# Kernel optimization log

Measured on AMD Instinct MI355X. Metric: run time of the kernel, lower is better.

## Reference

```python
import jax, jax.numpy as jnp
import numpy as np

N = 8192
EPS = 1e-6


def setup_inputs() -> dict:
    key = jax.random.key(0)
    k1, k2, k3, k4 = jax.random.split(key, 4)
    P_risk = jax.random.normal(k1, (N,), dtype=jnp.float32)
    P_surv = jax.random.normal(k2, (N,), dtype=jnp.float32)
    T = jax.random.uniform(k3, (N,), dtype=jnp.float32)
    E = jax.random.randint(k4, (N,), 0, 2, dtype=jnp.int32)
    return {"P_risk": P_risk, "P_surv": P_surv, "T": T, "E": E}


def _compute_loss(P, M, E_eff):
    # P: [N] log-hazards, M: [N, N] float mask, E_eff: [N] effective event weights
    P_exp = jnp.exp(P)
    # sum_j M[i, j] * exp(P[j])  -- masked risk-set sum as a matvec
    P_exp_sum = M @ P_exp
    log_ratio = jnp.log(P_exp / (P_exp_sum + EPS))
    return -jnp.sum(log_ratio * E_eff) / jnp.sum(E_eff)


def reference(P_risk, P_surv, T, E):
    Ef = E.astype(jnp.float32)
    # M_risk[i, j] = 1 if T[i] < T[j]
    M_risk = (T[:, None] < T[None, :]).astype(jnp.float32)
    # M_surv[i, j] = 1 if T[i] > T[j] and E[j] == 1
    M_surv = (T[:, None] > T[None, :]).astype(jnp.float32) * Ef[None, :]

    # mode='risk': E * (row of M_risk nonempty)
    E_risk = Ef * (jnp.sum(M_risk, axis=1) > 0).astype(jnp.float32)
    # mode='surv': just (row of M_surv nonempty)
    E_surv = (jnp.sum(M_surv, axis=1) > 0).astype(jnp.float32)

    loss_risk = _compute_loss(P_risk, M_risk, E_risk)
    loss_surv = _compute_loss(P_surv, M_surv, E_surv)
    return (loss_risk, loss_surv)
```

## Files before the change

kernel.cpp:

```cpp
#include <hip/hip_runtime.h>
#include <math.h>

#define NN 8192
#define EPSF 1e-6f
#define R 8
#define GX (NN / R)


__global__ __launch_bounds__(256) void ds_main(
    const float* __restrict__ Pr, const float* __restrict__ Ps,
    const float* __restrict__ T,  const int* __restrict__ E,
    float4* __restrict__ part) {
  const int tid  = threadIdx.x;
  const int row0 = blockIdx.x * R;

  float Ti[R];
#pragma unroll
  for (int r = 0; r < R; ++r) Ti[r] = T[row0 + r];

  float sr[R], ss[R];
#pragma unroll
  for (int r = 0; r < R; ++r) { sr[r] = 0.0f; ss[r] = 0.0f; }

  for (int k = 0; k < NN; k += 1024) {
    const int j = k + tid * 4;
    float4 t4  = *(const float4*)(T  + j);
    float4 pr4 = *(const float4*)(Pr + j);
    float4 ps4 = *(const float4*)(Ps + j);
    int4   e4  = *(const int4*)(E  + j);
    float er0 = __expf(pr4.x), er1 = __expf(pr4.y),
          er2 = __expf(pr4.z), er3 = __expf(pr4.w);
    float es0 = e4.x ? __expf(ps4.x) : 0.0f;
    float es1 = e4.y ? __expf(ps4.y) : 0.0f;
    float es2 = e4.z ? __expf(ps4.z) : 0.0f;
    float es3 = e4.w ? __expf(ps4.w) : 0.0f;
#pragma unroll
    for (int r = 0; r < R; ++r) {
      bool g0 = t4.x > Ti[r];  sr[r] += g0 ? er0 : 0.0f;  ss[r] += g0 ? 0.0f : es0;
      bool g1 = t4.y > Ti[r];  sr[r] += g1 ? er1 : 0.0f;  ss[r] += g1 ? 0.0f : es1;
      bool g2 = t4.z > Ti[r];  sr[r] += g2 ? er2 : 0.0f;  ss[r] += g2 ? 0.0f : es2;
      bool g3 = t4.w > Ti[r];  sr[r] += g3 ? er3 : 0.0f;  ss[r] += g3 ? 0.0f : es3;
    }
  }

#pragma unroll
  for (int r = 0; r < R; ++r) {
    for (int off = 32; off > 0; off >>= 1) {
      sr[r] += __shfl_down(sr[r], off);
      ss[r] += __shfl_down(ss[r], off);
    }
  }
  __shared__ float sh[4][2 * R];
  const int wid = tid >> 6, lane = tid & 63;
  if (lane == 0) {
#pragma unroll
    for (int r = 0; r < R; ++r) { sh[wid][r] = sr[r]; sh[wid][R + r] = ss[r]; }
  }
  __syncthreads();
  __shared__ float fin[2 * R];
  if (tid < 2 * R)
    fin[tid] = sh[0][tid] + sh[1][tid] + sh[2][tid] + sh[3][tid];
  __syncthreads();

  float nr = 0.0f, dr = 0.0f, ns = 0.0f, nds = 0.0f;
  if (tid < R) {
    const int   row = row0 + tid;
    const int   e   = E[row];
    const float prv = Pr[row], psv = Ps[row];
    const float es_diag = e ? __expf(psv) : 0.0f;
    const float srv = fin[tid];
    const float ssv = fin[R + tid] - es_diag;
    const float wr = (e != 0 && srv > 0.0f) ? 1.0f : 0.0f;
    const float wsv = (ssv > 0.0f) ? 1.0f : 0.0f;
    nr  = wr  * (prv - logf(srv + EPSF));
    dr  = wr;
    ns  = wsv * (psv - logf(ssv + EPSF));
    nds = wsv;
  }
  if (tid < 64) {
#pragma unroll
    for (int off = R / 2; off > 0; off >>= 1) {
      nr  += __shfl_down(nr,  off);
      dr  += __shfl_down(dr,  off);
      ns  += __shfl_down(ns,  off);
      nds += __shfl_down(nds, off);
    }
    if (tid == 0) part[blockIdx.x] = make_float4(nr, dr, ns, nds);
  }
}

__global__ __launch_bounds__(256) void ds_finalize(
    const float4* __restrict__ part, float* __restrict__ out) {
  float nr = 0.0f, dr = 0.0f, ns = 0.0f, nds = 0.0f;
  for (int i = threadIdx.x; i < GX; i += 256) {
    float4 p = part[i];
    nr += p.x; dr += p.y; ns += p.z; nds += p.w;
  }
  for (int off = 32; off > 0; off >>= 1) {
    nr  += __shfl_down(nr,  off);
    dr  += __shfl_down(dr,  off);
    ns  += __shfl_down(ns,  off);
    nds += __shfl_down(nds, off);
  }
  __shared__ float sh[4][4];
  const int wid = threadIdx.x >> 6, lane = threadIdx.x & 63;
  if (lane == 0) {
    sh[0][wid] = nr; sh[1][wid] = dr; sh[2][wid] = ns; sh[3][wid] = nds;
  }
  __syncthreads();
  if (threadIdx.x == 0) {
    float NR = sh[0][0] + sh[0][1] + sh[0][2] + sh[0][3];
    float DR = sh[1][0] + sh[1][1] + sh[1][2] + sh[1][3];
    float NS = sh[2][0] + sh[2][1] + sh[2][2] + sh[2][3];
    float DS = sh[3][0] + sh[3][1] + sh[3][2] + sh[3][3];
    out[0] = -NR / DR;
    out[1] = -NS / DS;
  }
}

extern "C" void kernel_launch(void* const* d_in, const int* in_sizes, int n_in,
                              void* d_out, int out_size, void* d_ws, size_t ws_size,
                              hipStream_t stream) {
  const float* Pr = (const float*)d_in[0];
  const float* Ps = (const float*)d_in[1];
  const float* T  = (const float*)d_in[2];
  const int*   E  = (const int*)d_in[3];
  float* out = (float*)d_out;

  float4* part = (float4*)d_ws;

  ds_main<<<GX, 256, 0, stream>>>(Pr, Ps, T, E, part);
  ds_finalize<<<1, 256, 0, stream>>>(part, out);
}
```

Measured before the change: 73.70 us.

## Replace quadratic masked risk-set sums with single-block bucket sort and prefix scans

The O(N^2) pairwise comparison over all rows is replaced by one workgroup that buckets samples by T into shared memory. It builds per-bucket exp sums with LDS atomics, takes prefix and suffix scans over the buckets, and scatters the samples into bucket order. Each element then needs only the scanned totals plus an exact comparison against the other members of its own bucket. The final reduction is folded into the same kernel, so the second launch disappears. The cost is a single-block design that relies on T being roughly uniform in [0,1) for bucket balance. Skewed T would still give correct results but would serialise the within-bucket loops.

```diff
diff --git a/kernel.cpp b/kernel.cpp
--- a/kernel.cpp
+++ b/kernel.cpp
@@ -1,118 +1,171 @@
 #include <hip/hip_runtime.h>
 #include <math.h>
 
-#define NN 8192
+#define NN   8192
+#define K    1024
+#define NT   1024
+#define EPT  8
 #define EPSF 1e-6f
-#define R 8
-#define GX (NN / R)
 
 
-__global__ __launch_bounds__(256) void ds_main(
+__device__ __forceinline__ float wave_incl_scan_f(float x, int lane) {
+#pragma unroll
+  for (int off = 1; off < 64; off <<= 1) {
+    float y = __shfl_up(x, off);
+    if (lane >= off) x += y;
+  }
+  return x;
+}
+__device__ __forceinline__ unsigned wave_incl_scan_u(unsigned x, int lane) {
+#pragma unroll
+  for (int off = 1; off < 64; off <<= 1) {
+    unsigned y = __shfl_up(x, off);
+    if (lane >= off) x += y;
+  }
+  return x;
+}
+
+__device__ __forceinline__ float block_excl_scan_f(float v, float* wtmp, int tid) {
+  const int lane = tid & 63, wid = tid >> 6;
+  float incl = wave_incl_scan_f(v, lane);
+  if (lane == 63) wtmp[wid] = incl;
+  __syncthreads();
+  if (tid < 64) {
+    float w = (tid < 16) ? wtmp[tid] : 0.0f;
+    w = wave_incl_scan_f(w, lane);
+    if (tid < 16) wtmp[tid] = w;
+  }
+  __syncthreads();
+  float base = (wid > 0) ? wtmp[wid - 1] : 0.0f;
+  return base + incl - v;
+}
+__device__ __forceinline__ unsigned block_excl_scan_u(unsigned v, unsigned* wtmp, int tid) {
+  const int lane = tid & 63, wid = tid >> 6;
+  unsigned incl = wave_incl_scan_u(v, lane);
+  if (lane == 63) wtmp[wid] = incl;
+  __syncthreads();
+  if (tid < 64) {
+    unsigned w = (tid < 16) ? wtmp[tid] : 0u;
+    w = wave_incl_scan_u(w, lane);
+    if (tid < 16) wtmp[tid] = w;
+  }
+  __syncthreads();
+  unsigned base = (wid > 0) ? wtmp[wid - 1] : 0u;
+  return base + incl - v;
+}
+
+__global__ __launch_bounds__(NT) void ds_all(
     const float* __restrict__ Pr, const float* __restrict__ Ps,
     const float* __restrict__ T,  const int* __restrict__ E,
-    float4* __restrict__ part) {
+    float* __restrict__ out) {
+  __shared__ unsigned cnt[K];
+  __shared__ unsigned cur[K];
+  __shared__ float    bER[K];
+  __shared__ float    bES[K];
+  __shared__ float    sT[NN];
+  __shared__ float    sER[NN];
+  __shared__ float    sES[NN];
+  __shared__ float    wtmp[64];
+
   const int tid  = threadIdx.x;
-  const int row0 = blockIdx.x * R;
+  const int lane = tid & 63, wid = tid >> 6;
 
-  float Ti[R];
+  cnt[tid] = 0u; cur[tid] = 0u; bER[tid] = 0.0f; bES[tid] = 0.0f;
+  __syncthreads();
+
+  float t8[EPT], pr8[EPT], ps8[EPT], er8[EPT], es8[EPT];
+  int   ev8[EPT], b8[EPT];
+  {
+    const int j = tid * EPT;
+    float4 ta = *(const float4*)(T  + j), tb = *(const float4*)(T  + j + 4);
+    float4 pa = *(const float4*)(Pr + j), pb = *(const float4*)(Pr + j + 4);
+    float4 qa = *(const float4*)(Ps + j), qb = *(const float4*)(Ps + j + 4);
+    int4   ea = *(const int4*)(E + j),    eb = *(const int4*)(E + j + 4);
+    t8[0]=ta.x;  t8[1]=ta.y;  t8[2]=ta.z;  t8[3]=ta.w;
+    t8[4]=tb.x;  t8[5]=tb.y;  t8[6]=tb.z;  t8[7]=tb.w;
+    pr8[0]=pa.x; pr8[1]=pa.y; pr8[2]=pa.z; pr8[3]=pa.w;
+    pr8[4]=pb.x; pr8[5]=pb.y; pr8[6]=pb.z; pr8[7]=pb.w;
+    ps8[0]=qa.x; ps8[1]=qa.y; ps8[2]=qa.z; ps8[3]=qa.w;
+    ps8[4]=qb.x; ps8[5]=qb.y; ps8[6]=qb.z; ps8[7]=qb.w;
+    ev8[0]=ea.x; ev8[1]=ea.y; ev8[2]=ea.z; ev8[3]=ea.w;
+    ev8[4]=eb.x; ev8[5]=eb.y; ev8[6]=eb.z; ev8[7]=eb.w;
+  }
 #pragma unroll
-  for (int r = 0; r < R; ++r) Ti[r] = T[row0 + r];
+  for (int e = 0; e < EPT; ++e) {
+    er8[e] = __expf(pr8[e]);
+    es8[e] = ev8[e] ? __expf(ps8[e]) : 0.0f;
+    int b = (int)(t8[e] * (float)K);
+    b = min(max(b, 0), K - 1);
+    b8[e] = b;
+    atomicAdd(&cnt[b], 1u);
+    atomicAdd(&bER[b], er8[e]);
+    atomicAdd(&bES[b], es8[e]);
+  }
+  __syncthreads();
 
-  float sr[R], ss[R];
+  unsigned myc  = cnt[tid];
+  float    myes = bES[tid];
+  float    myerR = bER[K - 1 - tid];
+  __syncthreads();
+  unsigned startv = block_excl_scan_u(myc, (unsigned*)wtmp, tid);
+  __syncthreads();
+  float prees = block_excl_scan_f(myes, wtmp, tid);
+  __syncthreads();
+  float sufR = block_excl_scan_f(myerR, wtmp, tid);
+  __syncthreads();
+  cnt[tid] = startv;
+  bES[tid] = prees;
+  bER[K - 1 - tid] = sufR;
+  __syncthreads();
+
 #pragma unroll
-  for (int r = 0; r < R; ++r) { sr[r] = 0.0f; ss[r] = 0.0f; }
+  for (int e = 0; e < EPT; ++e) {
+    unsigned pos = cnt[b8[e]] + atomicAdd(&cur[b8[e]], 1u);
+    sT[pos]  = t8[e];
+    sER[pos] = er8[e];
+    sES[pos] = es8[e];
+  }
+  __syncthreads();
 
-  for (int k = 0; k < NN; k += 1024) {
-    const int j = k + tid * 4;
-    float4 t4  = *(const float4*)(T  + j);
-    float4 pr4 = *(const float4*)(Pr + j);
-    float4 ps4 = *(const float4*)(Ps + j);
-    int4   e4  = *(const int4*)(E  + j);
-    float er0 = __expf(pr4.x), er1 = __expf(pr4.y),
-          er2 = __expf(pr4.z), er3 = __expf(pr4.w);
-    float es0 = e4.x ? __expf(ps4.x) : 0.0f;
-    float es1 = e4.y ? __expf(ps4.y) : 0.0f;
-    float es2 = e4.z ? __expf(ps4.z) : 0.0f;
-    float es3 = e4.w ? __expf(ps4.w) : 0.0f;
+  float nr = 0.0f, dr = 0.0f, ns = 0.0f, nds = 0.0f;
 #pragma unroll
-    for (int r = 0; r < R; ++r) {
-      bool g0 = t4.x > Ti[r];  sr[r] += g0 ? er0 : 0.0f;  ss[r] += g0 ? 0.0f : es0;
-      bool g1 = t4.y > Ti[r];  sr[r] += g1 ? er1 : 0.0f;  ss[r] += g1 ? 0.0f : es1;
-      bool g2 = t4.z > Ti[r];  sr[r] += g2 ? er2 : 0.0f;  ss[r] += g2 ? 0.0f : es2;
-      bool g3 = t4.w > Ti[r];  sr[r] += g3 ? er3 : 0.0f;  ss[r] += g3 ? 0.0f : es3;
+  for (int e = 0; e < EPT; ++e) {
+    const int   b = b8[e];
+    const float t = t8[e];
+    float srv = bER[b];
+    float ssv = bES[b];
+    const unsigned p0 = cnt[b];
+    const unsigned p1 = (b == K - 1) ? (unsigned)NN : cnt[b + 1];
+    for (unsigned p = p0; p < p1; ++p) {
+      float tj = sT[p];
+      srv += (tj > t) ? sER[p] : 0.0f;
+      ssv += (tj < t) ? sES[p] : 0.0f;
     }
+    const float wr  = (ev8[e] != 0 && srv > 0.0f) ? 1.0f : 0.0f;
+    const float wsv = (ssv > 0.0f) ? 1.0f : 0.0f;
+    nr  += wr  * (pr8[e] - logf(srv + EPSF));
+    dr  += wr;
+    ns  += wsv * (ps8[e] - logf(ssv + EPSF));
+    nds += wsv;
   }
 
 #pragma unroll
-  for (int r = 0; r < R; ++r) {
-    for (int off = 32; off > 0; off >>= 1) {
-      sr[r] += __shfl_down(sr[r], off);
-      ss[r] += __shfl_down(ss[r], off);
-    }
-  }
-  __shared__ float sh[4][2 * R];
-  const int wid = tid >> 6, lane = tid & 63;
-  if (lane == 0) {
-#pragma unroll
-    for (int r = 0; r < R; ++r) { sh[wid][r] = sr[r]; sh[wid][R + r] = ss[r]; }
-  }
-  __syncthreads();
-  __shared__ float fin[2 * R];
-  if (tid < 2 * R)
-    fin[tid] = sh[0][tid] + sh[1][tid] + sh[2][tid] + sh[3][tid];
-  __syncthreads();
-
-  float nr = 0.0f, dr = 0.0f, ns = 0.0f, nds = 0.0f;
-  if (tid < R) {
-    const int   row = row0 + tid;
-    const int   e   = E[row];
-    const float prv = Pr[row], psv = Ps[row];
-    const float es_diag = e ? __expf(psv) : 0.0f;
-    const float srv = fin[tid];
-    const float ssv = fin[R + tid] - es_diag;
-    const float wr = (e != 0 && srv > 0.0f) ? 1.0f : 0.0f;
-    const float wsv = (ssv > 0.0f) ? 1.0f : 0.0f;
-    nr  = wr  * (prv - logf(srv + EPSF));
-    dr  = wr;
-    ns  = wsv * (psv - logf(ssv + EPSF));
-    nds = wsv;
-  }
-  if (tid < 64) {
-#pragma unroll
-    for (int off = R / 2; off > 0; off >>= 1) {
-      nr  += __shfl_down(nr,  off);
-      dr  += __shfl_down(dr,  off);
-      ns  += __shfl_down(ns,  off);
-      nds += __shfl_down(nds, off);
-    }
-    if (tid == 0) part[blockIdx.x] = make_float4(nr, dr, ns, nds);
-  }
-}
-
-__global__ __launch_bounds__(256) void ds_finalize(
-    const float4* __restrict__ part, float* __restrict__ out) {
-  float nr = 0.0f, dr = 0.0f, ns = 0.0f, nds = 0.0f;
-  for (int i = threadIdx.x; i < GX; i += 256) {
-    float4 p = part[i];
-    nr += p.x; dr += p.y; ns += p.z; nds += p.w;
-  }
   for (int off = 32; off > 0; off >>= 1) {
     nr  += __shfl_down(nr,  off);
     dr  += __shfl_down(dr,  off);
     ns  += __shfl_down(ns,  off);
     nds += __shfl_down(nds, off);
   }
-  __shared__ float sh[4][4];
-  const int wid = threadIdx.x >> 6, lane = threadIdx.x & 63;
   if (lane == 0) {
-    sh[0][wid] = nr; sh[1][wid] = dr; sh[2][wid] = ns; sh[3][wid] = nds;
+    wtmp[wid] = nr; wtmp[16 + wid] = dr; wtmp[32 + wid] = ns; wtmp[48 + wid] = nds;
   }
   __syncthreads();
-  if (threadIdx.x == 0) {
-    float NR = sh[0][0] + sh[0][1] + sh[0][2] + sh[0][3];
-    float DR = sh[1][0] + sh[1][1] + sh[1][2] + sh[1][3];
-    float NS = sh[2][0] + sh[2][1] + sh[2][2] + sh[2][3];
-    float DS = sh[3][0] + sh[3][1] + sh[3][2] + sh[3][3];
+  if (tid == 0) {
+    float NR = 0, DR = 0, NS = 0, DS = 0;
+#pragma unroll
+    for (int w = 0; w < 16; ++w) {
+      NR += wtmp[w]; DR += wtmp[16 + w]; NS += wtmp[32 + w]; DS += wtmp[48 + w];
+    }
     out[0] = -NR / DR;
     out[1] = -NS / DS;
   }
@@ -127,8 +180,5 @@
   const int*   E  = (const int*)d_in[3];
   float* out = (float*)d_out;
 
-  float4* part = (float4*)d_ws;
-
-  ds_main<<<GX, 256, 0, stream>>>(Pr, Ps, T, E, part);
-  ds_finalize<<<1, 256, 0, stream>>>(part, out);
+  ds_all<<<1, NT, 0, stream>>>(Pr, Ps, T, E, out);
 }
```

Result: slower. 99.81 us (+35.4%).

## Split column range across two blocks per row group and move log-loss to finalize

Applied to the files above, without the earlier changes.

Each 8-row group is now handled by two blocks, each covering half of the j columns, which doubles the grid from 1024 to 2048 blocks. Per-row partial risk and survival sums go to workspace arrays. A 1024-thread finalize kernel then adds the two halves per row, subtracts the diagonal term, and computes the log-loss terms and reductions. The aim is more parallelism and occupancy (launch bounds now request 8 blocks per CU). In exchange the per-row log work moves into a single-block finalize pass that reads 4x8192 extra floats, and each block redoes the exp work for its half.

```diff
diff --git a/kernel.cpp b/kernel.cpp
--- a/kernel.cpp
+++ b/kernel.cpp
@@ -1,18 +1,24 @@
 #include <hip/hip_runtime.h>
 #include <math.h>
 
-#define NN 8192
+#define NN   8192
+#define R    8
+#define HALF (NN / 2)
+#define GX   ((NN / R) * 2)
+
 #define EPSF 1e-6f
-#define R 8
-#define GX (NN / R)
 
 
-__global__ __launch_bounds__(256) void ds_main(
+__global__ __launch_bounds__(256, 8) void ds_main(
     const float* __restrict__ Pr, const float* __restrict__ Ps,
     const float* __restrict__ T,  const int* __restrict__ E,
-    float4* __restrict__ part) {
-  const int tid  = threadIdx.x;
-  const int row0 = blockIdx.x * R;
+    float* __restrict__ sumR0, float* __restrict__ sumR1,
+    float* __restrict__ sumS0, float* __restrict__ sumS1) {
+  const int tid   = threadIdx.x;
+  const int g     = blockIdx.x >> 1;
+  const int h     = blockIdx.x & 1;
+  const int row0  = g * R;
+  const int jbase = h * HALF;
 
   float Ti[R];
 #pragma unroll
@@ -22,8 +28,8 @@
 #pragma unroll
   for (int r = 0; r < R; ++r) { sr[r] = 0.0f; ss[r] = 0.0f; }
 
-  for (int k = 0; k < NN; k += 1024) {
-    const int j = k + tid * 4;
+  for (int k = 0; k < HALF; k += 1024) {
+    const int j = jbase + k + tid * 4;
     float4 t4  = *(const float4*)(T  + j);
     float4 pr4 = *(const float4*)(Pr + j);
     float4 ps4 = *(const float4*)(Ps + j);
@@ -57,44 +63,34 @@
     for (int r = 0; r < R; ++r) { sh[wid][r] = sr[r]; sh[wid][R + r] = ss[r]; }
   }
   __syncthreads();
-  __shared__ float fin[2 * R];
-  if (tid < 2 * R)
-    fin[tid] = sh[0][tid] + sh[1][tid] + sh[2][tid] + sh[3][tid];
-  __syncthreads();
-
-  float nr = 0.0f, dr = 0.0f, ns = 0.0f, nds = 0.0f;
-  if (tid < R) {
-    const int   row = row0 + tid;
-    const int   e   = E[row];
-    const float prv = Pr[row], psv = Ps[row];
-    const float es_diag = e ? __expf(psv) : 0.0f;
-    const float srv = fin[tid];
-    const float ssv = fin[R + tid] - es_diag;
-    const float wr = (e != 0 && srv > 0.0f) ? 1.0f : 0.0f;
-    const float wsv = (ssv > 0.0f) ? 1.0f : 0.0f;
-    nr  = wr  * (prv - logf(srv + EPSF));
-    dr  = wr;
-    ns  = wsv * (psv - logf(ssv + EPSF));
-    nds = wsv;
-  }
-  if (tid < 64) {
-#pragma unroll
-    for (int off = R / 2; off > 0; off >>= 1) {
-      nr  += __shfl_down(nr,  off);
-      dr  += __shfl_down(dr,  off);
-      ns  += __shfl_down(ns,  off);
-      nds += __shfl_down(nds, off);
-    }
-    if (tid == 0) part[blockIdx.x] = make_float4(nr, dr, ns, nds);
+  if (tid < 2 * R) {
+    float v = sh[0][tid] + sh[1][tid] + sh[2][tid] + sh[3][tid];
+    float* SR = h ? sumR1 : sumR0;
+    float* SS = h ? sumS1 : sumS0;
+    if (tid < R) SR[row0 + tid] = v;
+    else         SS[row0 + (tid - R)] = v;
   }
 }
 
-__global__ __launch_bounds__(256) void ds_finalize(
-    const float4* __restrict__ part, float* __restrict__ out) {
+__global__ __launch_bounds__(1024) void ds_finalize(
+    const float* __restrict__ Pr, const float* __restrict__ Ps,
+    const int* __restrict__ E,
+    const float* __restrict__ sumR0, const float* __restrict__ sumR1,
+    const float* __restrict__ sumS0, const float* __restrict__ sumS1,
+    float* __restrict__ out) {
   float nr = 0.0f, dr = 0.0f, ns = 0.0f, nds = 0.0f;
-  for (int i = threadIdx.x; i < GX; i += 256) {
-    float4 p = part[i];
-    nr += p.x; dr += p.y; ns += p.z; nds += p.w;
+  for (int i = threadIdx.x; i < NN; i += 1024) {
+    const int e = E[i];
+    const float prv = Pr[i], psv = Ps[i];
+    const float es_diag = e ? __expf(psv) : 0.0f;
+    const float srv = sumR0[i] + sumR1[i];
+    const float ssv = (sumS0[i] + sumS1[i]) - es_diag;
+    const float wr  = (e != 0 && srv > 0.0f) ? 1.0f : 0.0f;
+    const float wsv = (ssv > 0.0f) ? 1.0f : 0.0f;
+    nr  += wr  * (prv - logf(srv + EPSF));
+    dr  += wr;
+    ns  += wsv * (psv - logf(ssv + EPSF));
+    nds += wsv;
   }
   for (int off = 32; off > 0; off >>= 1) {
     nr  += __shfl_down(nr,  off);
@@ -102,17 +98,18 @@
     ns  += __shfl_down(ns,  off);
     nds += __shfl_down(nds, off);
   }
-  __shared__ float sh[4][4];
+  __shared__ float sh[4][16];
   const int wid = threadIdx.x >> 6, lane = threadIdx.x & 63;
   if (lane == 0) {
     sh[0][wid] = nr; sh[1][wid] = dr; sh[2][wid] = ns; sh[3][wid] = nds;
   }
   __syncthreads();
   if (threadIdx.x == 0) {
-    float NR = sh[0][0] + sh[0][1] + sh[0][2] + sh[0][3];
-    float DR = sh[1][0] + sh[1][1] + sh[1][2] + sh[1][3];
-    float NS = sh[2][0] + sh[2][1] + sh[2][2] + sh[2][3];
-    float DS = sh[3][0] + sh[3][1] + sh[3][2] + sh[3][3];
+    float NR = 0, DR = 0, NS = 0, DS = 0;
+#pragma unroll
+    for (int w = 0; w < 16; ++w) {
+      NR += sh[0][w]; DR += sh[1][w]; NS += sh[2][w]; DS += sh[3][w];
+    }
     out[0] = -NR / DR;
     out[1] = -NS / DS;
   }
@@ -127,8 +124,12 @@
   const int*   E  = (const int*)d_in[3];
   float* out = (float*)d_out;
 
-  float4* part = (float4*)d_ws;
+  float* ws    = (float*)d_ws;
+  float* sumR0 = ws;
+  float* sumR1 = ws + NN;
+  float* sumS0 = ws + 2 * NN;
+  float* sumS1 = ws + 3 * NN;
 
-  ds_main<<<GX, 256, 0, stream>>>(Pr, Ps, T, E, part);
-  ds_finalize<<<1, 256, 0, stream>>>(part, out);
+  ds_main<<<GX, 256, 0, stream>>>(Pr, Ps, T, E, sumR0, sumR1, sumS0, sumS1);
+  ds_finalize<<<1, 1024, 0, stream>>>(Pr, Ps, E, sumR0, sumR1, sumS0, sumS1, out);
 }
```

New measurement: 75.96 us. 1.03x slower.
